# Kernel optimization log

Hardware: AMD Instinct MI355X
Metric: run time of the kernel (lower is better)

Reference implementation:

```python
import jax, jax.numpy as jnp
import numpy as np

TOTAL_NODES = 1048576
D_FEAT = 128
NUM_SEGMENTS = 16384


def setup_inputs() -> dict:
    key = jax.random.key(0)
    k1, k2 = jax.random.split(key)
    x = jax.random.normal(k1, (TOTAL_NODES, D_FEAT), dtype=jnp.float32)
    segment_ids = jnp.sort(
        jax.random.randint(k2, (TOTAL_NODES,), 0, NUM_SEGMENTS, dtype=jnp.int64)
    )
    return {"x": x, "segment_ids": segment_ids, "num_segments": NUM_SEGMENTS}


def reference(x, segment_ids, num_segments):
    # Fused multi-stat segmented reduction: per-graph max, min, mean, std
    # (torch default std is unbiased, correction=1), stacked as in
    # th.stack([max, min, mean, std]) -> output [num_graphs, 4, d_feat].
    n = x.shape[0]
    cnt = jax.ops.segment_sum(
        jnp.ones((n,), dtype=x.dtype), segment_ids,
        num_segments=num_segments, indices_are_sorted=True,
    )[:, None]  # [G, 1]
    s = jax.ops.segment_sum(x, segment_ids, num_segments=num_segments,
                            indices_are_sorted=True)          # [G, D]
    sq = jax.ops.segment_sum(x * x, segment_ids, num_segments=num_segments,
                             indices_are_sorted=True)         # [G, D]
    mx = jax.ops.segment_max(x, segment_ids, num_segments=num_segments,
                             indices_are_sorted=True)         # [G, D]
    mn = jax.ops.segment_min(x, segment_ids, num_segments=num_segments,
                             indices_are_sorted=True)         # [G, D]
    mean = s / cnt
    # unbiased variance: (sum(x^2) - n*mean^2) / (n - 1)
    var = (sq - cnt * mean * mean) / (cnt - 1.0)
    std = jnp.sqrt(jnp.maximum(var, 0.0))
    return jnp.stack([mx, mn, mean, std], axis=1)  # [G, 4, D]
```

## Files before the change

### kernel.cpp

```cpp
#include <hip/hip_runtime.h>
#include <math.h>

#define D_FEAT   128
#define NUM_SEG  16384

__device__ __forceinline__ float4 f4max(float4 a, float4 b) {
    return make_float4(fmaxf(a.x, b.x), fmaxf(a.y, b.y), fmaxf(a.z, b.z), fmaxf(a.w, b.w));
}
__device__ __forceinline__ float4 f4min(float4 a, float4 b) {
    return make_float4(fminf(a.x, b.x), fminf(a.y, b.y), fminf(a.z, b.z), fminf(a.w, b.w));
}
__device__ __forceinline__ float4 f4add(float4 a, float4 b) {
    return make_float4(a.x + b.x, a.y + b.y, a.z + b.z, a.w + b.w);
}

__global__ __launch_bounds__(256) void seg_bounds_kernel(
    const int* __restrict__ seg32, int* __restrict__ offs, int n)
{
    const int i = blockIdx.x * 256 + threadIdx.x;
    if (i >= n) return;
    const bool wide = (seg32[n - 1] == 0);
    int cur, prev;
    if (wide) {
        const long long* s = (const long long*)seg32;
        cur  = (int)s[i];
        prev = (i == 0) ? -1 : (int)s[i - 1];
    } else {
        cur  = seg32[i];
        prev = (i == 0) ? -1 : seg32[i - 1];
    }
    for (int g = prev + 1; g <= cur; ++g) offs[g] = i;
    if (i == n - 1) {
        for (int g = cur + 1; g <= NUM_SEG; ++g) offs[g] = n;
    }
}

__global__ __launch_bounds__(128) void seg_pool_kernel(
    const float* __restrict__ x,
    const int*   __restrict__ offs,
    float*       __restrict__ out)
{
    const int g = blockIdx.x;
    const int t = threadIdx.x;

    const int start = offs[g];
    const int end   = offs[g + 1];
    const int cnt   = end - start;

    const int ro = t >> 5;
    const int c4 = t & 31;

    float4 mx = make_float4(-INFINITY, -INFINITY, -INFINITY, -INFINITY);
    float4 mn = make_float4( INFINITY,  INFINITY,  INFINITY,  INFINITY);
    float4 sm = make_float4(0.f, 0.f, 0.f, 0.f);
    float4 sq = make_float4(0.f, 0.f, 0.f, 0.f);

    const float* xc = x + (c4 << 2);
    int r = start + ro;

    #define ACC(v) do {                         \
        mx = f4max(mx, (v));                    \
        mn = f4min(mn, (v));                    \
        sm = f4add(sm, (v));                    \
        sq.x = fmaf((v).x, (v).x, sq.x);        \
        sq.y = fmaf((v).y, (v).y, sq.y);        \
        sq.z = fmaf((v).z, (v).z, sq.z);        \
        sq.w = fmaf((v).w, (v).w, sq.w);        \
    } while (0)

    for (; r + 12 < end; r += 16) {
        const float4 v0 = *(const float4*)(xc + (size_t)(r     ) * D_FEAT);
        const float4 v1 = *(const float4*)(xc + (size_t)(r +  4) * D_FEAT);
        const float4 v2 = *(const float4*)(xc + (size_t)(r +  8) * D_FEAT);
        const float4 v3 = *(const float4*)(xc + (size_t)(r + 12) * D_FEAT);
        ACC(v0); ACC(v1); ACC(v2); ACC(v3);
    }
    for (; r < end; r += 4) {
        const float4 v = *(const float4*)(xc + (size_t)r * D_FEAT);
        ACC(v);
    }
    #undef ACC

    __shared__ float4 red[4][4][32];
    red[0][ro][c4] = mx;
    red[1][ro][c4] = mn;
    red[2][ro][c4] = sm;
    red[3][ro][c4] = sq;
    __syncthreads();

    if (t < 32) {
        float4 MX = red[0][0][t];
        float4 MN = red[1][0][t];
        float4 SM = red[2][0][t];
        float4 SQ = red[3][0][t];
        #pragma unroll
        for (int rr = 1; rr < 4; ++rr) {
            MX = f4max(MX, red[0][rr][t]);
            MN = f4min(MN, red[1][rr][t]);
            SM = f4add(SM, red[2][rr][t]);
            SQ = f4add(SQ, red[3][rr][t]);
        }

        const float fc    = (float)cnt;
        const float inv_c = 1.0f / fc;
        const float inv_m = 1.0f / (fc - 1.0f);

        float4 MEAN = make_float4(SM.x * inv_c, SM.y * inv_c, SM.z * inv_c, SM.w * inv_c);
        float4 STD;
        STD.x = sqrtf(fmaxf((SQ.x - fc * MEAN.x * MEAN.x) * inv_m, 0.0f));
        STD.y = sqrtf(fmaxf((SQ.y - fc * MEAN.y * MEAN.y) * inv_m, 0.0f));
        STD.z = sqrtf(fmaxf((SQ.z - fc * MEAN.z * MEAN.z) * inv_m, 0.0f));
        STD.w = sqrtf(fmaxf((SQ.w - fc * MEAN.w * MEAN.w) * inv_m, 0.0f));

        float* base = out + (size_t)g * 4 * D_FEAT + (t << 2);
        *(float4*)(base + 0 * D_FEAT) = MX;
        *(float4*)(base + 1 * D_FEAT) = MN;
        *(float4*)(base + 2 * D_FEAT) = MEAN;
        *(float4*)(base + 3 * D_FEAT) = STD;
    }
}

extern "C" void kernel_launch(void* const* d_in, const int* in_sizes, int n_in,
                              void* d_out, int out_size, void* d_ws, size_t ws_size,
                              hipStream_t stream) {
    const float* x   = (const float*)d_in[0];
    const int*   seg = (const int*)d_in[1];
    float*       out = (float*)d_out;
    int*         offs = (int*)d_ws;
    const int n = in_sizes[0] / D_FEAT;

    seg_bounds_kernel<<<(n + 255) / 256, 256, 0, stream>>>(seg, offs, n);
    seg_pool_kernel<<<NUM_SEG, 128, 0, stream>>>(x, offs, out);
}
```

Measured before the change: 679.4 us.

## Assign one wavefront per segment and drop shared-memory cross-row reduction

Each 64-lane wavefront now owns a whole segment, with each lane handling two features via float2 loads and walking every row. Four segments share one 256-thread block. This removes the LDS reduction and __syncthreads, and adds 16-row unrolled loads for memory-level parallelism. In exchange each lane issues narrower 8-byte loads, and per-wave serial row iteration lengthens for large segments.

```diff
diff --git a/kernel.cpp b/kernel.cpp
--- a/kernel.cpp
+++ b/kernel.cpp
@@ -1,18 +1,9 @@
 #include <hip/hip_runtime.h>
 #include <math.h>
 
-#define D_FEAT   128
-#define NUM_SEG  16384
-
-__device__ __forceinline__ float4 f4max(float4 a, float4 b) {
-    return make_float4(fmaxf(a.x, b.x), fmaxf(a.y, b.y), fmaxf(a.z, b.z), fmaxf(a.w, b.w));
-}
-__device__ __forceinline__ float4 f4min(float4 a, float4 b) {
-    return make_float4(fminf(a.x, b.x), fminf(a.y, b.y), fminf(a.z, b.z), fminf(a.w, b.w));
-}
-__device__ __forceinline__ float4 f4add(float4 a, float4 b) {
-    return make_float4(a.x + b.x, a.y + b.y, a.z + b.z, a.w + b.w);
-}
+#define D_FEAT      128
+#define NUM_SEG     16384
+#define SEG_PER_BLK 4
 
 __global__ __launch_bounds__(256) void seg_bounds_kernel(
     const int* __restrict__ seg32, int* __restrict__ offs, int n)
@@ -35,89 +26,70 @@
     }
 }
 
-__global__ __launch_bounds__(128) void seg_pool_kernel(
+__global__ __launch_bounds__(256) void seg_pool_kernel(
     const float* __restrict__ x,
     const int*   __restrict__ offs,
     float*       __restrict__ out)
 {
-    const int g = blockIdx.x;
-    const int t = threadIdx.x;
+    const int wave = threadIdx.x >> 6;
+    const int lane = threadIdx.x & 63;
+    const int g = blockIdx.x * SEG_PER_BLK + wave;
 
     const int start = offs[g];
     const int end   = offs[g + 1];
-    const int cnt   = end - start;
 
-    const int ro = t >> 5;
-    const int c4 = t & 31;
+    const float* xc = x + (lane << 1);
 
-    float4 mx = make_float4(-INFINITY, -INFINITY, -INFINITY, -INFINITY);
-    float4 mn = make_float4( INFINITY,  INFINITY,  INFINITY,  INFINITY);
-    float4 sm = make_float4(0.f, 0.f, 0.f, 0.f);
-    float4 sq = make_float4(0.f, 0.f, 0.f, 0.f);
+    float2 mx = make_float2(-INFINITY, -INFINITY);
+    float2 mn = make_float2( INFINITY,  INFINITY);
+    float2 sm = make_float2(0.f, 0.f);
+    float2 sq = make_float2(0.f, 0.f);
 
-    const float* xc = x + (c4 << 2);
-    int r = start + ro;
-
-    #define ACC(v) do {                         \
-        mx = f4max(mx, (v));                    \
-        mn = f4min(mn, (v));                    \
-        sm = f4add(sm, (v));                    \
-        sq.x = fmaf((v).x, (v).x, sq.x);        \
-        sq.y = fmaf((v).y, (v).y, sq.y);        \
-        sq.z = fmaf((v).z, (v).z, sq.z);        \
-        sq.w = fmaf((v).w, (v).w, sq.w);        \
+#define LDR(k) const float2 v##k = *(const float2*)(xc + (size_t)(r + (k)) * D_FEAT)
+#define ACC(v) do {                                                   \
+        mx.x = fmaxf(mx.x, (v).x);  mx.y = fmaxf(mx.y, (v).y);        \
+        mn.x = fminf(mn.x, (v).x);  mn.y = fminf(mn.y, (v).y);        \
+        sm.x += (v).x;              sm.y += (v).y;                    \
+        sq.x = fmaf((v).x, (v).x, sq.x);                              \
+        sq.y = fmaf((v).y, (v).y, sq.y);                              \
     } while (0)
 
-    for (; r + 12 < end; r += 16) {
-        const float4 v0 = *(const float4*)(xc + (size_t)(r     ) * D_FEAT);
-        const float4 v1 = *(const float4*)(xc + (size_t)(r +  4) * D_FEAT);
-        const float4 v2 = *(const float4*)(xc + (size_t)(r +  8) * D_FEAT);
-        const float4 v3 = *(const float4*)(xc + (size_t)(r + 12) * D_FEAT);
+    int r = start;
+    for (; r + 15 < end; r += 16) {
+        LDR(0);  LDR(1);  LDR(2);  LDR(3);
+        LDR(4);  LDR(5);  LDR(6);  LDR(7);
+        LDR(8);  LDR(9);  LDR(10); LDR(11);
+        LDR(12); LDR(13); LDR(14); LDR(15);
+        ACC(v0);  ACC(v1);  ACC(v2);  ACC(v3);
+        ACC(v4);  ACC(v5);  ACC(v6);  ACC(v7);
+        ACC(v8);  ACC(v9);  ACC(v10); ACC(v11);
+        ACC(v12); ACC(v13); ACC(v14); ACC(v15);
+    }
+    for (; r + 3 < end; r += 4) {
+        LDR(0); LDR(1); LDR(2); LDR(3);
         ACC(v0); ACC(v1); ACC(v2); ACC(v3);
     }
-    for (; r < end; r += 4) {
-        const float4 v = *(const float4*)(xc + (size_t)r * D_FEAT);
-        ACC(v);
+    for (; r < end; ++r) {
+        LDR(0);
+        ACC(v0);
     }
-    #undef ACC
+#undef LDR
+#undef ACC
 
-    __shared__ float4 red[4][4][32];
-    red[0][ro][c4] = mx;
-    red[1][ro][c4] = mn;
-    red[2][ro][c4] = sm;
-    red[3][ro][c4] = sq;
-    __syncthreads();
+    const float fc    = (float)(end - start);
+    const float inv_c = 1.0f / fc;
+    const float inv_m = 1.0f / (fc - 1.0f);
 
-    if (t < 32) {
-        float4 MX = red[0][0][t];
-        float4 MN = red[1][0][t];
-        float4 SM = red[2][0][t];
-        float4 SQ = red[3][0][t];
-        #pragma unroll
-        for (int rr = 1; rr < 4; ++rr) {
-            MX = f4max(MX, red[0][rr][t]);
-            MN = f4min(MN, red[1][rr][t]);
-            SM = f4add(SM, red[2][rr][t]);
-            SQ = f4add(SQ, red[3][rr][t]);
-        }
+    float2 mean = make_float2(sm.x * inv_c, sm.y * inv_c);
+    float2 stdv;
+    stdv.x = sqrtf(fmaxf((sq.x - fc * mean.x * mean.x) * inv_m, 0.0f));
+    stdv.y = sqrtf(fmaxf((sq.y - fc * mean.y * mean.y) * inv_m, 0.0f));
 
-        const float fc    = (float)cnt;
-        const float inv_c = 1.0f / fc;
-        const float inv_m = 1.0f / (fc - 1.0f);
-
-        float4 MEAN = make_float4(SM.x * inv_c, SM.y * inv_c, SM.z * inv_c, SM.w * inv_c);
-        float4 STD;
-        STD.x = sqrtf(fmaxf((SQ.x - fc * MEAN.x * MEAN.x) * inv_m, 0.0f));
-        STD.y = sqrtf(fmaxf((SQ.y - fc * MEAN.y * MEAN.y) * inv_m, 0.0f));
-        STD.z = sqrtf(fmaxf((SQ.z - fc * MEAN.z * MEAN.z) * inv_m, 0.0f));
-        STD.w = sqrtf(fmaxf((SQ.w - fc * MEAN.w * MEAN.w) * inv_m, 0.0f));
-
-        float* base = out + (size_t)g * 4 * D_FEAT + (t << 2);
-        *(float4*)(base + 0 * D_FEAT) = MX;
-        *(float4*)(base + 1 * D_FEAT) = MN;
-        *(float4*)(base + 2 * D_FEAT) = MEAN;
-        *(float4*)(base + 3 * D_FEAT) = STD;
-    }
+    float* base = out + (size_t)g * (4 * D_FEAT) + (lane << 1);
+    *(float2*)(base + 0 * D_FEAT) = mx;
+    *(float2*)(base + 1 * D_FEAT) = mn;
+    *(float2*)(base + 2 * D_FEAT) = mean;
+    *(float2*)(base + 3 * D_FEAT) = stdv;
 }
 
 extern "C" void kernel_launch(void* const* d_in, const int* in_sizes, int n_in,
@@ -130,5 +102,5 @@
     const int n = in_sizes[0] / D_FEAT;
 
     seg_bounds_kernel<<<(n + 255) / 256, 256, 0, stream>>>(seg, offs, n);
-    seg_pool_kernel<<<NUM_SEG, 128, 0, stream>>>(x, offs, out);
+    seg_pool_kernel<<<NUM_SEG / SEG_PER_BLK, 256, 0, stream>>>(x, offs, out);
 }
```

Result: slower. 696.2 us (+2.5%).
